# Optimization experiments

Hardware: AMD Instinct MI355X
Metric: run time of the kernel (lower is better)

The kernel has to match this reference:

```python
import jax, jax.numpy as jnp
import numpy as np

NEG_ATT = 0.2   # GATv2Conv internal leaky_relu slope
NEG_ACT = 0.01  # nn.LeakyReLU default slope (activation between layers)

def _segment_softmax(logits, seg, n):
    m = jax.ops.segment_max(logits, seg, num_segments=n)
    ex = jnp.exp(logits - m[seg])
    s = jax.ops.segment_sum(ex, seg, num_segments=n)
    return ex / s[seg]

def _gatv2(h, Wl, bl, Wr, br, att, bias, src, dst, n):
    # PyG GATv2Conv, heads=1: xl = lin_l(h) (source/message), xr = lin_r(h) (target)
    xl = h @ Wl + bl                                   # [N, H]
    xr = h @ Wr + br                                   # [N, H]
    e = jax.nn.leaky_relu(xl[src] + xr[dst], NEG_ATT)  # [E, H]
    logits = e @ att                                   # [E]
    alpha = _segment_softmax(logits, dst, n)           # softmax over incoming edges per dst
    out = jax.ops.segment_sum(xl[src] * alpha[:, None], dst, num_segments=n)
    return out + bias

def setup_inputs() -> dict:
    key = jax.random.key(0)
    G, P, DEG, DIN, H, EX, OUT, NC = 4096, 24, 8, 32, 128, 8, 3, 6
    N = G * P
    E = N * DEG
    ks = jax.random.split(key, 16)
    x = jax.random.normal(ks[0], (N, DIN), jnp.float32)
    gid = jnp.arange(E) // (P * DEG)  # edges stay within their graph
    src = gid * P + jax.random.randint(ks[1], (E,), 0, P)
    dst = gid * P + jax.random.randint(ks[2], (E,), 0, P)
    batch = jnp.repeat(jnp.arange(G), P)
    extra_feat = jax.random.normal(ks[3], (G, EX), jnp.float32)
    sc = lambda k, shp: jax.random.normal(k, shp, jnp.float32) * 0.05
    return dict(
        x=x, src=src, dst=dst, batch=batch, extra_feat=extra_feat,
        W_init0=sc(ks[4], (DIN, H)), b_init0=jnp.zeros((H,), jnp.float32),
        W_init1=sc(ks[5], (H, H)), b_init1=jnp.zeros((H,), jnp.float32),
        Wl=sc(ks[6], (NC, H, H)), bl=jnp.zeros((NC, H), jnp.float32),
        Wr=sc(ks[7], (NC, H, H)), br=jnp.zeros((NC, H), jnp.float32),
        att=sc(ks[8], (NC, H)), cbias=jnp.zeros((NC, H), jnp.float32),
        Wf0=sc(ks[9], (H + EX, H)), bf0=jnp.zeros((H,), jnp.float32),
        Wf1=sc(ks[10], (H, H)), bf1=jnp.zeros((H,), jnp.float32),
        Wf2=sc(ks[11], (H, OUT)), bf2=jnp.zeros((OUT,), jnp.float32),
    )

def reference(x, src, dst, batch, extra_feat,
              W_init0, b_init0, W_init1, b_init1,
              Wl, bl, Wr, br, att, cbias,
              Wf0, bf0, Wf1, bf1, Wf2, bf2):
    N = x.shape[0]
    G = extra_feat.shape[0]
    # init MLP
    h = jax.nn.leaky_relu(x @ W_init0 + b_init0, NEG_ACT)
    h = jax.nn.leaky_relu(h @ W_init1 + b_init1, NEG_ACT)
    # GATv2Conv adds self-loops
    loop = jnp.arange(N)
    src_sl = jnp.concatenate([src, loop])
    dst_sl = jnp.concatenate([dst, loop])
    NUM_GAT, MP = 2, 3
    for g in range(NUM_GAT):
        for m in range(MP):
            c = g * MP + m
            h = _gatv2(h, Wl[c], bl[c], Wr[c], br[c], att[c], cbias[c], src_sl, dst_sl, N)
            if m < MP - 1:  # BasicGNN: act between convs, not after last
                h = jax.nn.leaky_relu(h, NEG_ACT)
    # global_add_pool + extra features + final MLP
    pooled = jax.ops.segment_sum(h, batch, num_segments=G)
    z = jnp.concatenate([pooled, extra_feat], axis=1)
    z = jax.nn.leaky_relu(z @ Wf0 + bf0, NEG_ACT)
    z = jax.nn.leaky_relu(z @ Wf1 + bf1, NEG_ACT)
    return z @ Wf2 + bf2
```

## Files before the change

kernel.cpp:

```cpp
#include <hip/hip_runtime.h>

#define NG   4096
#define P    24
#define EPG  192
#define ESL  216
#define DIN  32
#define H    128
#define EX   8
#define NOUT 3
#define HSS  136

typedef short bf16x8 __attribute__((ext_vector_type(8)));
typedef float f32x4  __attribute__((ext_vector_type(4)));

__device__ __forceinline__ float bf2f(unsigned short u) {
    return __uint_as_float(((unsigned)u) << 16);
}
__device__ __forceinline__ unsigned short f2bf(float v) {
    unsigned u = __float_as_uint(v);
    unsigned r = u + 0x7fffu + ((u >> 16) & 1u);
    return (unsigned short)(r >> 16);
}
__device__ __forceinline__ float lrelu(float v, float s) { return v > 0.f ? v : v * s; }

__global__ void cvtw(const float* __restrict__ W0, const float* __restrict__ W1,
                     const float* __restrict__ Wl, const float* __restrict__ Wr,
                     unsigned short* __restrict__ ws) {
    int i = blockIdx.x * 256 + threadIdx.x;
    float v;
    if (i < 4096)            { int n = i >> 5, k = i & 31;  v = W0[k * 128 + n]; }
    else if (i < 20480)      { int j = i - 4096;  int n = j >> 7, k = j & 127; v = W1[k * 128 + n]; }
    else if (i < 118784)     { int j = i - 20480; int c = j >> 14, r = j & 16383;
                               int n = r >> 7, k = r & 127; v = Wl[c * 16384 + k * 128 + n]; }
    else if (i < 217088)     { int j = i - 118784; int c = j >> 14, r = j & 16383;
                               int n = r >> 7, k = r & 127; v = Wr[c * 16384 + k * 128 + n]; }
    else return;
    ws[i] = f2bf(v);
}

__global__ __launch_bounds__(256, 3) void gat_all(
    const float* __restrict__ x,
    const int*   __restrict__ src,
    const int*   __restrict__ dst,
    const float* __restrict__ extra,
    const float* __restrict__ b0,  const float* __restrict__ b1,
    const float* __restrict__ bl,  const float* __restrict__ br,
    const float* __restrict__ att, const float* __restrict__ cbias,
    const float* __restrict__ Wf0, const float* __restrict__ bf0,
    const float* __restrict__ Wf1, const float* __restrict__ bf1,
    const float* __restrict__ Wf2, const float* __restrict__ bf2,
    const unsigned short* __restrict__ wsb,
    float* __restrict__ out)
{
    __shared__ unsigned short hs [32 * HSS];
    __shared__ unsigned short xls[32 * HSS];
    __shared__ unsigned short xrs[32 * HSS];
    __shared__ unsigned short xlT[128 * 32];
    __shared__ float          Amat[1024];
    __shared__ unsigned short Amb [1024];
    __shared__ float att_s[H];
    __shared__ float dsum[P];
    __shared__ unsigned char es_[ESL], ed_[ESL];

    const int g    = blockIdx.x;
    const int t    = threadIdx.x;
    const int lane = t & 63;
    const int w    = t >> 6;
    const int m16  = lane & 15;
    const int kc   = lane >> 4;
    const long long gn = (long long)g * P;

    const unsigned short* W0T = wsb;
    const unsigned short* W1T = wsb + 4096;
    const unsigned short* WLT = wsb + 20480;
    const unsigned short* WRT = wsb + 118784;

    if (t < ESL) {
        int s, d;
        if (t < EPG) {
            s = src[(long long)g * EPG + t] - (int)gn;
            d = dst[(long long)g * EPG + t] - (int)gn;
        } else { s = d = t - EPG; }
        es_[t] = (unsigned char)s;
        ed_[t] = (unsigned char)d;
    }
    {
        unsigned short* xB = xlT;
        if (t < 192) {
            float4 v = *reinterpret_cast<const float4*>(&x[gn * DIN + t * 4]);
            ushort4 u = make_ushort4(f2bf(v.x), f2bf(v.y), f2bf(v.z), f2bf(v.w));
            *reinterpret_cast<ushort4*>(&xB[t * 4]) = u;
        } else {
            *reinterpret_cast<ushort4*>(&xB[768 + (t - 192) * 4]) = make_ushort4(0, 0, 0, 0);
        }
    }
    __syncthreads();

    {
        f32x4 acc[4] = {};
        bf16x8 a = *reinterpret_cast<const bf16x8*>(&xlT[((w & 1) * 16 + m16) * 32 + kc * 8]);
        #pragma unroll
        for (int i = 0; i < 4; ++i) {
            int nt = (w >> 1) * 4 + i;
            bf16x8 b = *reinterpret_cast<const bf16x8*>(&W0T[(nt * 16 + m16) * 32 + kc * 8]);
            acc[i] = __builtin_amdgcn_mfma_f32_16x16x32_bf16(a, b, acc[i], 0, 0, 0);
        }
        #pragma unroll
        for (int i = 0; i < 4; ++i) {
            int col = (w >> 1) * 64 + i * 16 + m16;
            float bv = b0[col];
            #pragma unroll
            for (int r = 0; r < 4; ++r) {
                int row = (w & 1) * 16 + kc * 4 + r;
                xls[row * HSS + col] = f2bf(lrelu(acc[i][r] + bv, 0.01f));
            }
        }
    }
    __syncthreads();

    {
        f32x4 acc[4] = {};
        for (int kt = 0; kt < 4; ++kt) {
            bf16x8 a = *reinterpret_cast<const bf16x8*>(&xls[((w & 1) * 16 + m16) * HSS + kt * 32 + kc * 8]);
            #pragma unroll
            for (int i = 0; i < 4; ++i) {
                int nt = (w >> 1) * 4 + i;
                bf16x8 b = *reinterpret_cast<const bf16x8*>(&W1T[(nt * 16 + m16) * 128 + kt * 32 + kc * 8]);
                acc[i] = __builtin_amdgcn_mfma_f32_16x16x32_bf16(a, b, acc[i], 0, 0, 0);
            }
        }
        #pragma unroll
        for (int i = 0; i < 4; ++i) {
            int col = (w >> 1) * 64 + i * 16 + m16;
            float bv = b1[col];
            #pragma unroll
            for (int r = 0; r < 4; ++r) {
                int row = (w & 1) * 16 + kc * 4 + r;
                hs[row * HSS + col] = f2bf(lrelu(acc[i][r] + bv, 0.01f));
            }
        }
    }
    __syncthreads();

    for (int c = 0; c < 6; ++c) {
        if (t < H)  att_s[t] = att[c * H + t];
        if (t < P)  dsum[t] = 0.f;
        *reinterpret_cast<float4*>(&Amat[t * 4]) = make_float4(0.f, 0.f, 0.f, 0.f);

        const unsigned short* WT   = ((w & 1) ? WRT : WLT) + c * 16384;
        const float*          bias = ((w & 1) ? br : bl) + c * H;
        f32x4 acc[8] = {};
        for (int kt = 0; kt < 4; ++kt) {
            bf16x8 a0 = *reinterpret_cast<const bf16x8*>(&hs[(m16)      * HSS + kt * 32 + kc * 8]);
            bf16x8 a1 = *reinterpret_cast<const bf16x8*>(&hs[(16 + m16) * HSS + kt * 32 + kc * 8]);
            #pragma unroll
            for (int i = 0; i < 4; ++i) {
                int nt = (w >> 1) * 4 + i;
                bf16x8 b = *reinterpret_cast<const bf16x8*>(&WT[(nt * 16 + m16) * 128 + kt * 32 + kc * 8]);
                acc[i]     = __builtin_amdgcn_mfma_f32_16x16x32_bf16(a0, b, acc[i],     0, 0, 0);
                acc[4 + i] = __builtin_amdgcn_mfma_f32_16x16x32_bf16(a1, b, acc[4 + i], 0, 0, 0);
            }
        }
        {
            unsigned short* XO = (w & 1) ? xrs : xls;
            const bool isL = !(w & 1);
            #pragma unroll
            for (int mt = 0; mt < 2; ++mt)
            #pragma unroll
            for (int i = 0; i < 4; ++i) {
                int col = (w >> 1) * 64 + i * 16 + m16;
                float bv = bias[col];
                #pragma unroll
                for (int r = 0; r < 4; ++r) {
                    int row = mt * 16 + kc * 4 + r;
                    unsigned short ub = f2bf(acc[mt * 4 + i][r] + bv);
                    XO[row * HSS + col] = ub;
                    if (isL) xlT[col * 32 + row] = ub;
                }
            }
        }
        __syncthreads();

        float ex = 0.f; int sd_s = 0, sd_d = 0;
        if (t < ESL) {
            sd_s = es_[t]; sd_d = ed_[t];
            const unsigned short* xa = &xls[sd_s * HSS];
            const unsigned short* xb = &xrs[sd_d * HSS];
            float lg = 0.f;
            for (int cc = 0; cc < 16; ++cc) {
                bf16x8 a = *reinterpret_cast<const bf16x8*>(&xa[cc * 8]);
                bf16x8 b = *reinterpret_cast<const bf16x8*>(&xb[cc * 8]);
                #pragma unroll
                for (int q = 0; q < 8; ++q) {
                    float u = bf2f((unsigned short)a[q]) + bf2f((unsigned short)b[q]);
                    u = lrelu(u, 0.2f);
                    lg += u * att_s[cc * 8 + q];
                }
            }
            ex = __expf(lg);
            atomicAdd(&dsum[sd_d], ex);
        }
        __syncthreads();
        if (t < ESL) {
            float alpha = ex / dsum[sd_d];
            atomicAdd(&Amat[sd_d * 32 + sd_s], alpha);
        }
        __syncthreads();
        {
            float4 v = *reinterpret_cast<const float4*>(&Amat[t * 4]);
            ushort4 u = make_ushort4(f2bf(v.x), f2bf(v.y), f2bf(v.z), f2bf(v.w));
            *reinterpret_cast<ushort4*>(&Amb[t * 4]) = u;
        }
        __syncthreads();

        {
            f32x4 acc2[4] = {};
            bf16x8 a = *reinterpret_cast<const bf16x8*>(&Amb[((w & 1) * 16 + m16) * 32 + kc * 8]);
            #pragma unroll
            for (int i = 0; i < 4; ++i) {
                int nt = (w >> 1) * 4 + i;
                bf16x8 b = *reinterpret_cast<const bf16x8*>(&xlT[(nt * 16 + m16) * 32 + kc * 8]);
                acc2[i] = __builtin_amdgcn_mfma_f32_16x16x32_bf16(a, b, acc2[i], 0, 0, 0);
            }
            const bool doact = (c % 3) < 2;
            #pragma unroll
            for (int i = 0; i < 4; ++i) {
                int col = (w >> 1) * 64 + i * 16 + m16;
                float cb = cbias[c * H + col];
                #pragma unroll
                for (int r = 0; r < 4; ++r) {
                    int row = (w & 1) * 16 + kc * 4 + r;
                    float v = acc2[i][r] + cb;
                    if (doact) v = lrelu(v, 0.01f);
                    hs[row * HSS + col] = f2bf(v);
                }
            }
        }
        __syncthreads();
    }

    float* z  = Amat;
    float* pa = Amat + 144;
    float* pb = Amat + 288;
    float* h1 = Amat + 432;
    float* qa = Amat + 576;
    float* qb = Amat + 720;
    float* h2 = Amat + 864;
    if (t < H) {
        float s = 0.f;
        for (int r = 0; r < P; ++r) s += bf2f(hs[r * HSS + t]);
        z[t] = s;
    } else if (t < H + EX) {
        z[t] = extra[(long long)g * EX + (t - H)];
    }
    __syncthreads();
    {
        int j = t & 127, half = t >> 7;
        float a = half ? 0.f : bf0[j];
        int k0 = half ? 68 : 0, k1 = half ? 136 : 68;
        for (int k = k0; k < k1; ++k) a += z[k] * Wf0[k * H + j];
        (half ? pb : pa)[j] = a;
    }
    __syncthreads();
    if (t < H) h1[t] = lrelu(pa[t] + pb[t], 0.01f);
    __syncthreads();
    {
        int j = t & 127, half = t >> 7;
        float a = half ? 0.f : bf1[j];
        int k0 = half * 64, k1 = k0 + 64;
        for (int k = k0; k < k1; ++k) a += h1[k] * Wf1[k * H + j];
        (half ? qb : qa)[j] = a;
    }
    __syncthreads();
    if (t < H) h2[t] = lrelu(qa[t] + qb[t], 0.01f);
    __syncthreads();
    if (t < NOUT) {
        float a = bf2[t];
        for (int k = 0; k < H; ++k) a += h2[k] * Wf2[k * NOUT + t];
        out[(long long)g * NOUT + t] = a;
    }
}

extern "C" void kernel_launch(void* const* d_in, const int* in_sizes, int n_in,
                              void* d_out, int out_size, void* d_ws, size_t ws_size,
                              hipStream_t stream) {
    (void)in_sizes; (void)n_in; (void)out_size; (void)ws_size;
    const float* x     = (const float*)d_in[0];
    const int*   src   = (const int*)  d_in[1];
    const int*   dst   = (const int*)  d_in[2];
    const float* extra = (const float*)d_in[4];
    const float* W0    = (const float*)d_in[5];
    const float* b0    = (const float*)d_in[6];
    const float* W1    = (const float*)d_in[7];
    const float* b1    = (const float*)d_in[8];
    const float* Wl    = (const float*)d_in[9];
    const float* bl    = (const float*)d_in[10];
    const float* Wr    = (const float*)d_in[11];
    const float* br    = (const float*)d_in[12];
    const float* att   = (const float*)d_in[13];
    const float* cbias = (const float*)d_in[14];
    const float* Wf0   = (const float*)d_in[15];
    const float* bf0   = (const float*)d_in[16];
    const float* Wf1   = (const float*)d_in[17];
    const float* bf1   = (const float*)d_in[18];
    const float* Wf2   = (const float*)d_in[19];
    const float* bf2   = (const float*)d_in[20];
    unsigned short* wsb = (unsigned short*)d_ws;
    float* out = (float*)d_out;

    cvtw<<<848, 256, 0, stream>>>(W0, W1, Wl, Wr, wsb);
    gat_all<<<NG, 256, 0, stream>>>(x, src, dst, extra, b0, b1, bl, br, att, cbias,
                                    Wf0, bf0, Wf1, bf1, Wf2, bf2, wsb, out);
}
```

Measured before the change: 449.8 us.

## Decompose leaky-relu attention logits into per-node dots plus abs term

Uses leaky_relu(u)=0.6u+0.4|u| so the per-edge logit becomes 0.6 times precomputed per-node att·xl and att·xr dot products plus 0.4 times an abs-weighted sum, with idle threads computing the node dots. It also pads the transposed xl buffer to a 40-element stride with vectorized stores, keeps edge indices in registers, drops the separate bf16 copy of the alpha matrix by converting on MFMA load, and raises launch bounds occupancy to 4 blocks. These aim to cut per-edge ALU work, LDS bank conflicts, one sync, and LDS footprint. The changed accumulation order alters rounding, and the higher occupancy target may increase register pressure.

```diff
diff --git a/kernel.cpp b/kernel.cpp
--- a/kernel.cpp
+++ b/kernel.cpp
@@ -9,13 +9,12 @@
 #define EX   8
 #define NOUT 3
 #define HSS  136
+#define XTS  40
 
 typedef short bf16x8 __attribute__((ext_vector_type(8)));
 typedef float f32x4  __attribute__((ext_vector_type(4)));
 
-__device__ __forceinline__ float bf2f(unsigned short u) {
-    return __uint_as_float(((unsigned)u) << 16);
-}
+__device__ __forceinline__ float u2f(unsigned u) { return __uint_as_float(u); }
 __device__ __forceinline__ unsigned short f2bf(float v) {
     unsigned u = __float_as_uint(v);
     unsigned r = u + 0x7fffu + ((u >> 16) & 1u);
@@ -38,7 +37,23 @@
     ws[i] = f2bf(v);
 }
 
-__global__ __launch_bounds__(256, 3) void gat_all(
+#define EDGE_PAIR(wa, wb, p, q)                                   \
+    do {                                                          \
+        float a0_ = u2f((wa) << 16);                              \
+        float a1_ = u2f((wa) & 0xffff0000u);                      \
+        float b0_ = u2f((wb) << 16);                              \
+        float b1_ = u2f((wb) & 0xffff0000u);                      \
+        abss = fmaf(fabsf(a0_ + b0_), (p), abss);                 \
+        abss = fmaf(fabsf(a1_ + b1_), (q), abss);                 \
+    } while (0)
+
+#define DOT_PAIR(wv, p, q)                                        \
+    do {                                                          \
+        sum = fmaf(u2f((wv) << 16), (p), sum);                    \
+        sum = fmaf(u2f((wv) & 0xffff0000u), (q), sum);            \
+    } while (0)
+
+__global__ __launch_bounds__(256, 4) void gat_all(
     const float* __restrict__ x,
     const int*   __restrict__ src,
     const int*   __restrict__ dst,
@@ -52,15 +67,15 @@
     const unsigned short* __restrict__ wsb,
     float* __restrict__ out)
 {
-    __shared__ unsigned short hs [32 * HSS];
-    __shared__ unsigned short xls[32 * HSS];
-    __shared__ unsigned short xrs[32 * HSS];
-    __shared__ unsigned short xlT[128 * 32];
-    __shared__ float          Amat[1024];
-    __shared__ unsigned short Amb [1024];
-    __shared__ float att_s[H];
-    __shared__ float dsum[P];
-    __shared__ unsigned char es_[ESL], ed_[ESL];
+    __shared__ __align__(16) unsigned short hb [32 * HSS];
+    __shared__ __align__(16) unsigned short xlb[32 * HSS];
+    __shared__ __align__(16) unsigned short xrb[32 * HSS];
+    __shared__ __align__(16) unsigned short xlT[128 * XTS];
+    __shared__ __align__(16) float          Am[1024];
+    __shared__ __align__(16) float          att_s[H];
+
+    float* dsum = Am + 768;
+    float* slr  = Am + 792;
 
     const int g    = blockIdx.x;
     const int t    = threadIdx.x;
@@ -75,30 +90,29 @@
     const unsigned short* WLT = wsb + 20480;
     const unsigned short* WRT = wsb + 118784;
 
+    int s_e = 0, d_e = 0;
     if (t < ESL) {
-        int s, d;
         if (t < EPG) {
-            s = src[(long long)g * EPG + t] - (int)gn;
-            d = dst[(long long)g * EPG + t] - (int)gn;
-        } else { s = d = t - EPG; }
-        es_[t] = (unsigned char)s;
-        ed_[t] = (unsigned char)d;
-    }
-    {
-        unsigned short* xB = xlT;
-        if (t < 192) {
-            float4 v = *reinterpret_cast<const float4*>(&x[gn * DIN + t * 4]);
-            ushort4 u = make_ushort4(f2bf(v.x), f2bf(v.y), f2bf(v.z), f2bf(v.w));
-            *reinterpret_cast<ushort4*>(&xB[t * 4]) = u;
-        } else {
-            *reinterpret_cast<ushort4*>(&xB[768 + (t - 192) * 4]) = make_ushort4(0, 0, 0, 0);
-        }
+            s_e = src[(long long)g * EPG + t] - (int)gn;
+            d_e = dst[(long long)g * EPG + t] - (int)gn;
+        } else { s_e = d_e = t - EPG; }
+    }
+
+    if (t < 192) {
+        float4 v = *reinterpret_cast<const float4*>(&x[gn * DIN + t * 4]);
+        int n = t >> 3, k = (t & 7) * 4;
+        *reinterpret_cast<ushort4*>(&xlT[n * XTS + k]) =
+            make_ushort4(f2bf(v.x), f2bf(v.y), f2bf(v.z), f2bf(v.w));
+    } else {
+        int u = t - 192;
+        int r = 24 + (u >> 3), k = (u & 7) * 4;
+        *reinterpret_cast<ushort4*>(&xlT[r * XTS + k]) = make_ushort4(0, 0, 0, 0);
     }
     __syncthreads();
 
     {
         f32x4 acc[4] = {};
-        bf16x8 a = *reinterpret_cast<const bf16x8*>(&xlT[((w & 1) * 16 + m16) * 32 + kc * 8]);
+        bf16x8 a = *reinterpret_cast<const bf16x8*>(&xlT[((w & 1) * 16 + m16) * XTS + kc * 8]);
         #pragma unroll
         for (int i = 0; i < 4; ++i) {
             int nt = (w >> 1) * 4 + i;
@@ -112,7 +126,7 @@
             #pragma unroll
             for (int r = 0; r < 4; ++r) {
                 int row = (w & 1) * 16 + kc * 4 + r;
-                xls[row * HSS + col] = f2bf(lrelu(acc[i][r] + bv, 0.01f));
+                xlb[row * HSS + col] = f2bf(lrelu(acc[i][r] + bv, 0.01f));
             }
         }
     }
@@ -121,7 +135,7 @@
     {
         f32x4 acc[4] = {};
         for (int kt = 0; kt < 4; ++kt) {
-            bf16x8 a = *reinterpret_cast<const bf16x8*>(&xls[((w & 1) * 16 + m16) * HSS + kt * 32 + kc * 8]);
+            bf16x8 a = *reinterpret_cast<const bf16x8*>(&xlb[((w & 1) * 16 + m16) * HSS + kt * 32 + kc * 8]);
             #pragma unroll
             for (int i = 0; i < 4; ++i) {
                 int nt = (w >> 1) * 4 + i;
@@ -136,23 +150,23 @@
             #pragma unroll
             for (int r = 0; r < 4; ++r) {
                 int row = (w & 1) * 16 + kc * 4 + r;
-                hs[row * HSS + col] = f2bf(lrelu(acc[i][r] + bv, 0.01f));
+                hb[row * HSS + col] = f2bf(lrelu(acc[i][r] + bv, 0.01f));
             }
         }
     }
     __syncthreads();
 
     for (int c = 0; c < 6; ++c) {
-        if (t < H)  att_s[t] = att[c * H + t];
-        if (t < P)  dsum[t] = 0.f;
-        *reinterpret_cast<float4*>(&Amat[t * 4]) = make_float4(0.f, 0.f, 0.f, 0.f);
+        if (t < H)   att_s[t] = att[c * H + t];
+        if (t < 192) *reinterpret_cast<float4*>(&Am[t * 4]) = make_float4(0.f, 0.f, 0.f, 0.f);
+        if (t < P)   dsum[t] = 0.f;
 
         const unsigned short* WT   = ((w & 1) ? WRT : WLT) + c * 16384;
         const float*          bias = ((w & 1) ? br : bl) + c * H;
         f32x4 acc[8] = {};
         for (int kt = 0; kt < 4; ++kt) {
-            bf16x8 a0 = *reinterpret_cast<const bf16x8*>(&hs[(m16)      * HSS + kt * 32 + kc * 8]);
-            bf16x8 a1 = *reinterpret_cast<const bf16x8*>(&hs[(16 + m16) * HSS + kt * 32 + kc * 8]);
+            bf16x8 a0 = *reinterpret_cast<const bf16x8*>(&hb[(m16)      * HSS + kt * 32 + kc * 8]);
+            bf16x8 a1 = *reinterpret_cast<const bf16x8*>(&hb[(16 + m16) * HSS + kt * 32 + kc * 8]);
             #pragma unroll
             for (int i = 0; i < 4; ++i) {
                 int nt = (w >> 1) * 4 + i;
@@ -162,7 +176,7 @@
             }
         }
         {
-            unsigned short* XO = (w & 1) ? xrs : xls;
+            unsigned short* XO = (w & 1) ? xrb : xlb;
             const bool isL = !(w & 1);
             #pragma unroll
             for (int mt = 0; mt < 2; ++mt)
@@ -170,56 +184,80 @@
             for (int i = 0; i < 4; ++i) {
                 int col = (w >> 1) * 64 + i * 16 + m16;
                 float bv = bias[col];
+                unsigned short ub[4];
                 #pragma unroll
                 for (int r = 0; r < 4; ++r) {
                     int row = mt * 16 + kc * 4 + r;
-                    unsigned short ub = f2bf(acc[mt * 4 + i][r] + bv);
-                    XO[row * HSS + col] = ub;
-                    if (isL) xlT[col * 32 + row] = ub;
+                    ub[r] = f2bf(acc[mt * 4 + i][r] + bv);
+                    XO[row * HSS + col] = ub[r];
                 }
-            }
-        }
-        __syncthreads();
-
-        float ex = 0.f; int sd_s = 0, sd_d = 0;
+                if (isL)
+                    *reinterpret_cast<ushort4*>(&xlT[col * XTS + mt * 16 + kc * 4]) =
+                        make_ushort4(ub[0], ub[1], ub[2], ub[3]);
+            }
+        }
+        __syncthreads();
+
+        float abss = 0.f;
         if (t < ESL) {
-            sd_s = es_[t]; sd_d = ed_[t];
-            const unsigned short* xa = &xls[sd_s * HSS];
-            const unsigned short* xb = &xrs[sd_d * HSS];
-            float lg = 0.f;
+            const uint4*  xa = reinterpret_cast<const uint4*>(&xlb[s_e * HSS]);
+            const uint4*  xb = reinterpret_cast<const uint4*>(&xrb[d_e * HSS]);
+            const float4* ap = reinterpret_cast<const float4*>(att_s);
+            #pragma unroll 4
             for (int cc = 0; cc < 16; ++cc) {
-                bf16x8 a = *reinterpret_cast<const bf16x8*>(&xa[cc * 8]);
-                bf16x8 b = *reinterpret_cast<const bf16x8*>(&xb[cc * 8]);
-                #pragma unroll
-                for (int q = 0; q < 8; ++q) {
-                    float u = bf2f((unsigned short)a[q]) + bf2f((unsigned short)b[q]);
-                    u = lrelu(u, 0.2f);
-                    lg += u * att_s[cc * 8 + q];
+                uint4 wa = xa[cc], wb = xb[cc];
+                float4 p0 = ap[cc * 2], p1 = ap[cc * 2 + 1];
+                EDGE_PAIR(wa.x, wb.x, p0.x, p0.y);
+                EDGE_PAIR(wa.y, wb.y, p0.z, p0.w);
+                EDGE_PAIR(wa.z, wb.z, p1.x, p1.y);
+                EDGE_PAIR(wa.w, wb.w, p1.z, p1.w);
+            }
+        } else {
+            int u = t - ESL;
+            const float4* ap = reinterpret_cast<const float4*>(att_s);
+            for (int task = u; task < 48; task += 40) {
+                int node = task >> 1;
+                const uint4* rp = reinterpret_cast<const uint4*>(
+                    ((task & 1) ? xrb : xlb) + node * HSS);
+                float sum = 0.f;
+                #pragma unroll 4
+                for (int cc = 0; cc < 16; ++cc) {
+                    uint4 wv = rp[cc];
+                    float4 p0 = ap[cc * 2], p1 = ap[cc * 2 + 1];
+                    DOT_PAIR(wv.x, p0.x, p0.y);
+                    DOT_PAIR(wv.y, p0.z, p0.w);
+                    DOT_PAIR(wv.z, p1.x, p1.y);
+                    DOT_PAIR(wv.w, p1.z, p1.w);
                 }
-            }
+                slr[task] = sum;
+            }
+        }
+        __syncthreads();
+
+        float ex = 0.f;
+        if (t < ESL) {
+            float lg = 0.4f * abss + 0.6f * (slr[2 * s_e] + slr[2 * d_e + 1]);
             ex = __expf(lg);
-            atomicAdd(&dsum[sd_d], ex);
-        }
-        __syncthreads();
-        if (t < ESL) {
-            float alpha = ex / dsum[sd_d];
-            atomicAdd(&Amat[sd_d * 32 + sd_s], alpha);
-        }
-        __syncthreads();
+            atomicAdd(&dsum[d_e], ex);
+        }
+        __syncthreads();
+        if (t < ESL) atomicAdd(&Am[d_e * 32 + s_e], ex / dsum[d_e]);
+        __syncthreads();
+
         {
-            float4 v = *reinterpret_cast<const float4*>(&Amat[t * 4]);
-            ushort4 u = make_ushort4(f2bf(v.x), f2bf(v.y), f2bf(v.z), f2bf(v.w));
-            *reinterpret_cast<ushort4*>(&Amb[t * 4]) = u;
-        }
-        __syncthreads();
-
-        {
+            int arow = (w & 1) * 16 + m16;
+            float4 u0 = *reinterpret_cast<const float4*>(&Am[arow * 32 + kc * 8]);
+            float4 u1 = *reinterpret_cast<const float4*>(&Am[arow * 32 + kc * 8 + 4]);
+            bf16x8 a;
+            a[0] = (short)f2bf(u0.x); a[1] = (short)f2bf(u0.y);
+            a[2] = (short)f2bf(u0.z); a[3] = (short)f2bf(u0.w);
+            a[4] = (short)f2bf(u1.x); a[5] = (short)f2bf(u1.y);
+            a[6] = (short)f2bf(u1.z); a[7] = (short)f2bf(u1.w);
             f32x4 acc2[4] = {};
-            bf16x8 a = *reinterpret_cast<const bf16x8*>(&Amb[((w & 1) * 16 + m16) * 32 + kc * 8]);
             #pragma unroll
             for (int i = 0; i < 4; ++i) {
                 int nt = (w >> 1) * 4 + i;
-                bf16x8 b = *reinterpret_cast<const bf16x8*>(&xlT[(nt * 16 + m16) * 32 + kc * 8]);
+                bf16x8 b = *reinterpret_cast<const bf16x8*>(&xlT[(nt * 16 + m16) * XTS + kc * 8]);
                 acc2[i] = __builtin_amdgcn_mfma_f32_16x16x32_bf16(a, b, acc2[i], 0, 0, 0);
             }
             const bool doact = (c % 3) < 2;
@@ -232,23 +270,23 @@
                     int row = (w & 1) * 16 + kc * 4 + r;
                     float v = acc2[i][r] + cb;
                     if (doact) v = lrelu(v, 0.01f);
-                    hs[row * HSS + col] = f2bf(v);
+                    hb[row * HSS + col] = f2bf(v);
                 }
             }
         }
         __syncthreads();
     }
 
-    float* z  = Amat;
-    float* pa = Amat + 144;
-    float* pb = Amat + 288;
-    float* h1 = Amat + 432;
-    float* qa = Amat + 576;
-    float* qb = Amat + 720;
-    float* h2 = Amat + 864;
+    float* z  = Am;
+    float* pa = Am + 144;
+    float* pb = Am + 288;
+    float* h1 = Am + 432;
+    float* qa = Am + 576;
+    float* qb = Am + 720;
+    float* h2 = Am + 864;
     if (t < H) {
         float s = 0.f;
-        for (int r = 0; r < P; ++r) s += bf2f(hs[r * HSS + t]);
+        for (int r = 0; r < P; ++r) s += u2f(((unsigned)hb[r * HSS + t]) << 16);
         z[t] = s;
     } else if (t < H + EX) {
         z[t] = extra[(long long)g * EX + (t - H)];
```

After: 394.6 us. 12.3% less time.
